# Kernel optimization log

Hardware: AMD Instinct MI355X
Metric: run time of the kernel (lower is better)

The kernel has to match this reference:

```python
import jax, jax.numpy as jnp
import numpy as np

OUTPUT_SIZE = 7
SPATIAL_SCALE = 0.25
SAMPLING_RATIO = 2


def setup_inputs() -> dict:
    key = jax.random.key(0)
    k1, k2, k3, k4, k5 = jax.random.split(key, 5)
    B, C, H, W = 4, 256, 100, 152
    N = 1000
    inp = jax.random.normal(k1, (B, C, H, W), dtype=jnp.float32)
    # image-space canvas is (H/scale, W/scale) = (400, 608); build valid xyxy boxes
    img_h, img_w = H / SPATIAL_SCALE, W / SPATIAL_SCALE
    x1 = jax.random.uniform(k2, (N,), minval=0.0, maxval=img_w - 16.0)
    y1 = jax.random.uniform(k3, (N,), minval=0.0, maxval=img_h - 16.0)
    bw = jax.random.uniform(k4, (N, 2), minval=8.0, maxval=160.0)
    x2 = jnp.minimum(x1 + bw[:, 0], img_w - 1.0)
    y2 = jnp.minimum(y1 + bw[:, 1], img_h - 1.0)
    boxes = jnp.stack([x1, y1, x2, y2], axis=1).astype(jnp.float32)
    box_indices = jax.random.randint(k5, (N,), 0, B, dtype=jnp.int32)
    return {"input": inp, "boxes": boxes, "box_indices": box_indices}


def _roi_align(feat, boxes, box_indices, P, scale, sr):
    # feat: [B,C,H,W], boxes: [N,4] xyxy in image coords, box_indices: [N]
    B, C, H, W = feat.shape
    N = boxes.shape[0]
    S = P * sr  # samples per side

    x1, y1, x2, y2 = [boxes[:, i] * scale for i in range(4)]
    roi_w = jnp.maximum(x2 - x1, 1.0)  # legacy aligned=False: min size 1
    roi_h = jnp.maximum(y2 - y1, 1.0)
    bin_w = roi_w / P
    bin_h = roi_h / P

    # sample s in [0,S): coord = start + bin * (s + 0.5)/sr  (== ph*bin + (iy+0.5)*bin/sr)
    offs = (jnp.arange(S, dtype=feat.dtype) + 0.5) / sr  # [S]
    ys = y1[:, None] + bin_h[:, None] * offs  # [N,S]
    xs = x1[:, None] + bin_w[:, None] * offs  # [N,S]

    valid_y = (ys > -1.0) & (ys < H)  # [N,S]
    valid_x = (xs > -1.0) & (xs < W)
    mask = (valid_y[:, :, None] & valid_x[:, None, :]).astype(feat.dtype)  # [N,S,S]

    yc = jnp.clip(ys, 0.0, H - 1)
    xc = jnp.clip(xs, 0.0, W - 1)
    yl = jnp.floor(yc).astype(jnp.int32)
    xl = jnp.floor(xc).astype(jnp.int32)
    yh = jnp.minimum(yl + 1, H - 1)
    xh = jnp.minimum(xl + 1, W - 1)
    ly = yc - yl  # [N,S]
    lx = xc - xl
    hy = 1.0 - ly
    hx = 1.0 - lx

    b = box_indices[:, None, None]  # [N,1,1]

    def corner(yi, xi):
        # gather [N,S,S,C] from feat[B,C,H,W]
        return feat[b, :, yi[:, :, None], xi[:, None, :]]

    w1 = (hy[:, :, None] * hx[:, None, :] * mask)[..., None]
    w2 = (hy[:, :, None] * lx[:, None, :] * mask)[..., None]
    w3 = (ly[:, :, None] * hx[:, None, :] * mask)[..., None]
    w4 = (ly[:, :, None] * lx[:, None, :] * mask)[..., None]

    vals = (w1 * corner(yl, xl) + w2 * corner(yl, xh)
            + w3 * corner(yh, xl) + w4 * corner(yh, xh))  # [N,S,S,C]

    # average pool sr x sr samples per bin
    pooled = vals.reshape(N, P, sr, P, sr, C).mean(axis=(2, 4))  # [N,P,P,C]
    return jnp.transpose(pooled, (0, 3, 1, 2))  # [N,C,P,P]


def reference(input, boxes, box_indices):
    return _roi_align(input, boxes, box_indices, OUTPUT_SIZE, SPATIAL_SCALE, SAMPLING_RATIO)
```

## Files before the change

### kernel.cpp

```cpp
#include <hip/hip_runtime.h>
#include <hip/hip_bf16.h>

#define BB    4
#define CC    256
#define HH    100
#define WW    152
#define NBOX  1000
#define PB    7
#define SRR   2
#define SCALE 0.25f

__global__ __launch_bounds__(1024) void order_kernel(
    const float* __restrict__ boxes, const int* __restrict__ inds,
    int* __restrict__ order)
{
    __shared__ unsigned cnt[256];
    __shared__ unsigned base[256];
    const int t = threadIdx.x;
    if (t < 256) cnt[t] = 0;
    __syncthreads();

    int key = 0;
    if (t < NBOX) {
        const float xc = 0.5f * (boxes[t * 4 + 0] + boxes[t * 4 + 2]) * SCALE;
        const float yc = 0.5f * (boxes[t * 4 + 1] + boxes[t * 4 + 3]) * SCALE;
        int xq = min((int)(xc * (8.0f / WW)), 7);
        int yq = min((int)(yc * (8.0f / HH)), 7);
        xq = max(xq, 0); yq = max(yq, 0);
        const int m = ((yq >> 2) & 1) << 5 | ((xq >> 2) & 1) << 4 |
                      ((yq >> 1) & 1) << 3 | ((xq >> 1) & 1) << 2 |
                      (yq & 1) << 1 | (xq & 1);
        key = (inds[t] << 6) | m;
        atomicAdd(&cnt[key], 1u);
    }
    __syncthreads();
    if (t < 256) base[t] = cnt[t];
    __syncthreads();
    for (int off = 1; off < 256; off <<= 1) {
        unsigned v = 0;
        if (t < 256 && t >= off) v = base[t - off];
        __syncthreads();
        if (t < 256) base[t] += v;
        __syncthreads();
    }
    if (t < 256) base[t] -= cnt[t];
    __syncthreads();
    if (t < 256) cnt[t] = 0;
    __syncthreads();
    if (t < NBOX) {
        const unsigned p = base[key] + atomicAdd(&cnt[key], 1u);
        order[p] = t;
    }
}

__global__ __launch_bounds__(256) void transpose_kernel(
    const float* __restrict__ in, ushort* __restrict__ out)
{
    __shared__ float tile[32][33];
    const int S = HH * WW;
    const int tilesS = S / 32;
    const int tilesC = CC / 32;

    int bid = blockIdx.x;
    int b   = bid / (tilesS * tilesC);
    int r   = bid % (tilesS * tilesC);
    int ts  = r / tilesC;
    int tc  = r % tilesC;
    int s0  = ts * 32, c0 = tc * 32;

    int tx  = threadIdx.x & 31;
    int ty4 = threadIdx.x >> 5;

    #pragma unroll
    for (int i = 0; i < 4; i++) {
        int c = c0 + ty4 * 4 + i;
        int s = s0 + tx;
        tile[ty4 * 4 + i][tx] = in[((size_t)b * CC + c) * S + s];
    }
    __syncthreads();
    #pragma unroll
    for (int i = 0; i < 4; i++) {
        int s = s0 + ty4 * 4 + i;
        int c = c0 + tx;
        __hip_bfloat16 h = __float2bfloat16(tile[tx][ty4 * 4 + i]);
        out[((size_t)b * S + s) * CC + c] = *(ushort*)&h;
    }
}

__global__ __launch_bounds__(512) void roialign_kernel(
    const ushort* __restrict__ feat,
    const float*  __restrict__ boxes,
    const int*    __restrict__ inds,
    const int*    __restrict__ order,
    float*        __restrict__ out)
{
    __shared__ float lds[128 * PB * PB];

    const int rank = (blockIdx.x & 7) * (2 * NBOX / 8) + (blockIdx.x >> 3);
    const int n    = order[rank >> 1];
    const int half = rank & 1;

    const int t = threadIdx.x;
    const int w = t >> 6;
    const int cl = 2 * (t & 63);

    const float x1 = boxes[n * 4 + 0] * SCALE;
    const float y1 = boxes[n * 4 + 1] * SCALE;
    const float x2 = boxes[n * 4 + 2] * SCALE;
    const float y2 = boxes[n * 4 + 3] * SCALE;
    const int   b  = inds[n];

    const float roi_w = fmaxf(x2 - x1, 1.0f);
    const float roi_h = fmaxf(y2 - y1, 1.0f);
    const float bin_w = roi_w * (1.0f / PB);
    const float bin_h = roi_h * (1.0f / PB);

    const ushort* fbase = feat + (size_t)b * (HH * WW * CC) + half * 128 + cl;
    const float inv = 1.0f / (SRR * SRR);

#define POS_BODY(P)                                                           \
    {                                                                         \
        const int py = (P) / PB;                                              \
        const int px = (P) % PB;                                              \
        float accx = 0.f, accy = 0.f;                                         \
        _Pragma("unroll")                                                     \
        for (int iy = 0; iy < SRR; iy++) {                                    \
            const float yy = y1 + bin_h * (((float)(py * SRR + iy) + 0.5f) * (1.0f / SRR)); \
            const bool  vy = (yy > -1.0f) && (yy < (float)HH);                \
            const float ycl = fminf(fmaxf(yy, 0.0f), (float)(HH - 1));        \
            const int   yl  = (int)ycl;                                       \
            const int   yh  = min(yl + 1, HH - 1);                            \
            const float lyf = ycl - (float)yl;                                \
            const float hyf = 1.0f - lyf;                                     \
            _Pragma("unroll")                                                 \
            for (int ix = 0; ix < SRR; ix++) {                                \
                const float xx = x1 + bin_w * (((float)(px * SRR + ix) + 0.5f) * (1.0f / SRR)); \
                const bool  vx = (xx > -1.0f) && (xx < (float)WW);            \
                const float m  = (vy && vx) ? 1.0f : 0.0f;                    \
                const float xcl = fminf(fmaxf(xx, 0.0f), (float)(WW - 1));    \
                const int   xl  = (int)xcl;                                   \
                const int   xh  = min(xl + 1, WW - 1);                        \
                const float lxf = xcl - (float)xl;                            \
                const float hxf = 1.0f - lxf;                                 \
                const float w11 = m * hyf * hxf;                              \
                const float w12 = m * hyf * lxf;                              \
                const float w21 = m * lyf * hxf;                              \
                const float w22 = m * lyf * lxf;                              \
                const uint v11 = *(const uint*)(fbase + (yl * WW + xl) * CC); \
                const uint v12 = *(const uint*)(fbase + (yl * WW + xh) * CC); \
                const uint v21 = *(const uint*)(fbase + (yh * WW + xl) * CC); \
                const uint v22 = *(const uint*)(fbase + (yh * WW + xh) * CC); \
                accx += w11 * __uint_as_float(v11 << 16)                      \
                      + w12 * __uint_as_float(v12 << 16)                      \
                      + w21 * __uint_as_float(v21 << 16)                      \
                      + w22 * __uint_as_float(v22 << 16);                     \
                accy += w11 * __uint_as_float(v11 & 0xFFFF0000u)              \
                      + w12 * __uint_as_float(v12 & 0xFFFF0000u)              \
                      + w21 * __uint_as_float(v21 & 0xFFFF0000u)              \
                      + w22 * __uint_as_float(v22 & 0xFFFF0000u);             \
            }                                                                 \
        }                                                                     \
        lds[(cl + 0) * (PB * PB) + (P)] = accx * inv;                         \
        lds[(cl + 1) * (PB * PB) + (P)] = accy * inv;                         \
    }

    #pragma unroll
    for (int it = 0; it < 3; it++) {
        const int p0 = w + 16 * it;
        POS_BODY(p0);
        POS_BODY(p0 + 8);
    }
    if (w == 0) POS_BODY(48);
#undef POS_BODY

    __syncthreads();
    float4*       out4 = (float4*)(out + ((size_t)n * CC + half * 128) * (PB * PB));
    const float4* lds4 = (const float4*)lds;
    #pragma unroll
    for (int k = t; k < (128 * PB * PB) / 4; k += 512)
        out4[k] = lds4[k];
}

extern "C" void kernel_launch(void* const* d_in, const int* in_sizes, int n_in,
                              void* d_out, int out_size, void* d_ws, size_t ws_size,
                              hipStream_t stream)
{
    const float* feat  = (const float*)d_in[0];
    const float* boxes = (const float*)d_in[1];
    const int*   inds  = (const int*)d_in[2];
    float*       out   = (float*)d_out;

    ushort* ft    = (ushort*)d_ws;
    int*    order = (int*)((char*)d_ws + (size_t)BB * HH * WW * CC * 2);

    order_kernel<<<1, 1024, 0, stream>>>(boxes, inds, order);
    const int tiles = BB * ((HH * WW) / 32) * (CC / 32);
    transpose_kernel<<<tiles, 256, 0, stream>>>(feat, ft);
    roialign_kernel<<<2 * NBOX, 512, 0, stream>>>(ft, boxes, inds, order, out);
}
```

Before: 54.61 us.

## Drop box ordering, process all channels per block, stage output in bf16 LDS

Removes the spatial/batch box-sorting kernel and its launch, assigning one block per box that covers all 256 channels with 8-byte loads (4 channels per thread) instead of two half-channel blocks. The LDS staging buffer now holds bf16 values, rounding the pooled results to bf16 before they are written out as fp32. This cuts a kernel launch and halves the block count. It loses the locality ordering and adds an extra rounding of the output, which changes numerics.

```diff
diff --git a/kernel.cpp b/kernel.cpp
--- a/kernel.cpp
+++ b/kernel.cpp
@@ -9,49 +9,6 @@
 #define PB    7
 #define SRR   2
 #define SCALE 0.25f
-
-__global__ __launch_bounds__(1024) void order_kernel(
-    const float* __restrict__ boxes, const int* __restrict__ inds,
-    int* __restrict__ order)
-{
-    __shared__ unsigned cnt[256];
-    __shared__ unsigned base[256];
-    const int t = threadIdx.x;
-    if (t < 256) cnt[t] = 0;
-    __syncthreads();
-
-    int key = 0;
-    if (t < NBOX) {
-        const float xc = 0.5f * (boxes[t * 4 + 0] + boxes[t * 4 + 2]) * SCALE;
-        const float yc = 0.5f * (boxes[t * 4 + 1] + boxes[t * 4 + 3]) * SCALE;
-        int xq = min((int)(xc * (8.0f / WW)), 7);
-        int yq = min((int)(yc * (8.0f / HH)), 7);
-        xq = max(xq, 0); yq = max(yq, 0);
-        const int m = ((yq >> 2) & 1) << 5 | ((xq >> 2) & 1) << 4 |
-                      ((yq >> 1) & 1) << 3 | ((xq >> 1) & 1) << 2 |
-                      (yq & 1) << 1 | (xq & 1);
-        key = (inds[t] << 6) | m;
-        atomicAdd(&cnt[key], 1u);
-    }
-    __syncthreads();
-    if (t < 256) base[t] = cnt[t];
-    __syncthreads();
-    for (int off = 1; off < 256; off <<= 1) {
-        unsigned v = 0;
-        if (t < 256 && t >= off) v = base[t - off];
-        __syncthreads();
-        if (t < 256) base[t] += v;
-        __syncthreads();
-    }
-    if (t < 256) base[t] -= cnt[t];
-    __syncthreads();
-    if (t < 256) cnt[t] = 0;
-    __syncthreads();
-    if (t < NBOX) {
-        const unsigned p = base[key] + atomicAdd(&cnt[key], 1u);
-        order[p] = t;
-    }
-}
 
 __global__ __launch_bounds__(256) void transpose_kernel(
     const float* __restrict__ in, ushort* __restrict__ out)
@@ -91,18 +48,14 @@
     const ushort* __restrict__ feat,
     const float*  __restrict__ boxes,
     const int*    __restrict__ inds,
-    const int*    __restrict__ order,
     float*        __restrict__ out)
 {
-    __shared__ float lds[128 * PB * PB];
+    __shared__ ushort lbuf[CC * PB * PB];
 
-    const int rank = (blockIdx.x & 7) * (2 * NBOX / 8) + (blockIdx.x >> 3);
-    const int n    = order[rank >> 1];
-    const int half = rank & 1;
-
+    const int n = blockIdx.x;
     const int t = threadIdx.x;
     const int w = t >> 6;
-    const int cl = 2 * (t & 63);
+    const int c0 = 4 * (t & 63);
 
     const float x1 = boxes[n * 4 + 0] * SCALE;
     const float y1 = boxes[n * 4 + 1] * SCALE;
@@ -115,14 +68,17 @@
     const float bin_w = roi_w * (1.0f / PB);
     const float bin_h = roi_h * (1.0f / PB);
 
-    const ushort* fbase = feat + (size_t)b * (HH * WW * CC) + half * 128 + cl;
+    const ushort* fbase = feat + (size_t)b * (HH * WW * CC) + c0;
     const float inv = 1.0f / (SRR * SRR);
+
+#define LO(u) __uint_as_float((u) << 16)
+#define HI(u) __uint_as_float((u) & 0xFFFF0000u)
 
 #define POS_BODY(P)                                                           \
     {                                                                         \
         const int py = (P) / PB;                                              \
         const int px = (P) % PB;                                              \
-        float accx = 0.f, accy = 0.f;                                         \
+        float a0 = 0.f, a1 = 0.f, a2 = 0.f, a3 = 0.f;                         \
         _Pragma("unroll")                                                     \
         for (int iy = 0; iy < SRR; iy++) {                                    \
             const float yy = y1 + bin_h * (((float)(py * SRR + iy) + 0.5f) * (1.0f / SRR)); \
@@ -146,22 +102,24 @@
                 const float w12 = m * hyf * lxf;                              \
                 const float w21 = m * lyf * hxf;                              \
                 const float w22 = m * lyf * lxf;                              \
-                const uint v11 = *(const uint*)(fbase + (yl * WW + xl) * CC); \
-                const uint v12 = *(const uint*)(fbase + (yl * WW + xh) * CC); \
-                const uint v21 = *(const uint*)(fbase + (yh * WW + xl) * CC); \
-                const uint v22 = *(const uint*)(fbase + (yh * WW + xh) * CC); \
-                accx += w11 * __uint_as_float(v11 << 16)                      \
-                      + w12 * __uint_as_float(v12 << 16)                      \
-                      + w21 * __uint_as_float(v21 << 16)                      \
-                      + w22 * __uint_as_float(v22 << 16);                     \
-                accy += w11 * __uint_as_float(v11 & 0xFFFF0000u)              \
-                      + w12 * __uint_as_float(v12 & 0xFFFF0000u)              \
-                      + w21 * __uint_as_float(v21 & 0xFFFF0000u)              \
-                      + w22 * __uint_as_float(v22 & 0xFFFF0000u);             \
+                const uint2 v11 = *(const uint2*)(fbase + (yl * WW + xl) * CC); \
+                const uint2 v12 = *(const uint2*)(fbase + (yl * WW + xh) * CC); \
+                const uint2 v21 = *(const uint2*)(fbase + (yh * WW + xl) * CC); \
+                const uint2 v22 = *(const uint2*)(fbase + (yh * WW + xh) * CC); \
+                a0 += w11 * LO(v11.x) + w12 * LO(v12.x) + w21 * LO(v21.x) + w22 * LO(v22.x); \
+                a1 += w11 * HI(v11.x) + w12 * HI(v12.x) + w21 * HI(v21.x) + w22 * HI(v22.x); \
+                a2 += w11 * LO(v11.y) + w12 * LO(v12.y) + w21 * LO(v21.y) + w22 * LO(v22.y); \
+                a3 += w11 * HI(v11.y) + w12 * HI(v12.y) + w21 * HI(v21.y) + w22 * HI(v22.y); \
             }                                                                 \
         }                                                                     \
-        lds[(cl + 0) * (PB * PB) + (P)] = accx * inv;                         \
-        lds[(cl + 1) * (PB * PB) + (P)] = accy * inv;                         \
+        __hip_bfloat16 h0 = __float2bfloat16(a0 * inv);                       \
+        __hip_bfloat16 h1 = __float2bfloat16(a1 * inv);                       \
+        __hip_bfloat16 h2 = __float2bfloat16(a2 * inv);                       \
+        __hip_bfloat16 h3 = __float2bfloat16(a3 * inv);                       \
+        lbuf[(c0 + 0) * (PB * PB) + (P)] = *(ushort*)&h0;                     \
+        lbuf[(c0 + 1) * (PB * PB) + (P)] = *(ushort*)&h1;                     \
+        lbuf[(c0 + 2) * (PB * PB) + (P)] = *(ushort*)&h2;                     \
+        lbuf[(c0 + 3) * (PB * PB) + (P)] = *(ushort*)&h3;                     \
     }
 
     #pragma unroll
@@ -172,13 +130,22 @@
     }
     if (w == 0) POS_BODY(48);
 #undef POS_BODY
+#undef LO
+#undef HI
 
     __syncthreads();
-    float4*       out4 = (float4*)(out + ((size_t)n * CC + half * 128) * (PB * PB));
-    const float4* lds4 = (const float4*)lds;
+    const uint2* l2   = (const uint2*)lbuf;
+    float4*      out4 = (float4*)(out + (size_t)n * (CC * PB * PB));
     #pragma unroll
-    for (int k = t; k < (128 * PB * PB) / 4; k += 512)
-        out4[k] = lds4[k];
+    for (int k = t; k < (CC * PB * PB) / 4; k += 512) {
+        const uint2 v = l2[k];
+        float4 o;
+        o.x = __uint_as_float(v.x << 16);
+        o.y = __uint_as_float(v.x & 0xFFFF0000u);
+        o.z = __uint_as_float(v.y << 16);
+        o.w = __uint_as_float(v.y & 0xFFFF0000u);
+        out4[k] = o;
+    }
 }
 
 extern "C" void kernel_launch(void* const* d_in, const int* in_sizes, int n_in,
@@ -190,11 +157,8 @@
     const int*   inds  = (const int*)d_in[2];
     float*       out   = (float*)d_out;
 
-    ushort* ft    = (ushort*)d_ws;
-    int*    order = (int*)((char*)d_ws + (size_t)BB * HH * WW * CC * 2);
-
-    order_kernel<<<1, 1024, 0, stream>>>(boxes, inds, order);
+    ushort* ft = (ushort*)d_ws;
     const int tiles = BB * ((HH * WW) / 32) * (CC / 32);
     transpose_kernel<<<tiles, 256, 0, stream>>>(feat, ft);
-    roialign_kernel<<<2 * NBOX, 512, 0, stream>>>(ft, boxes, inds, order, out);
+    roialign_kernel<<<NBOX, 512, 0, stream>>>(ft, boxes, inds, out);
 }
```

Result: faster. 52.52 us (-3.8%).
